# Optimization experiments

Measured on AMD Instinct MI355X. Metric: run time of the kernel, lower is better.

Reference implementation:

```python
import jax, jax.numpy as jnp
import numpy as np
from math import sqrt

D_MODEL = 512
HEADS = 8
D_K = D_MODEL // HEADS
DIM_FFN = 2048
EPS = 1e-6


def setup_inputs() -> dict:
    key = jax.random.key(0)
    ks = jax.random.split(key, 16)
    b, s = 2, 256
    inp = {
        "x": jax.random.normal(ks[0], (b, s, D_MODEL), dtype=jnp.float32),
        "connection_bias_k": jax.random.normal(ks[1], (b, s, s, D_MODEL), dtype=jnp.float32) * 0.02,
        "connection_bias_v": jax.random.normal(ks[2], (b, s, s, D_MODEL), dtype=jnp.float32) * 0.02,
        "mask": jnp.zeros((b, s), dtype=jnp.int32),
        "Wq": jax.random.normal(ks[3], (D_MODEL, D_MODEL), dtype=jnp.float32) / sqrt(D_MODEL),
        "bq": jnp.zeros((D_MODEL,), dtype=jnp.float32),
        "Wk": jax.random.normal(ks[4], (D_MODEL, D_MODEL), dtype=jnp.float32) / sqrt(D_MODEL),
        "bk": jnp.zeros((D_MODEL,), dtype=jnp.float32),
        "Wv": jax.random.normal(ks[5], (D_MODEL, D_MODEL), dtype=jnp.float32) / sqrt(D_MODEL),
        "bv": jnp.zeros((D_MODEL,), dtype=jnp.float32),
        "Wo": jax.random.normal(ks[6], (D_MODEL, D_MODEL), dtype=jnp.float32) / sqrt(D_MODEL),
        "bo": jnp.zeros((D_MODEL,), dtype=jnp.float32),
        "alpha1": jnp.ones((D_MODEL,), dtype=jnp.float32),
        "beta1": jnp.zeros((D_MODEL,), dtype=jnp.float32),
        "alpha2": jnp.ones((D_MODEL,), dtype=jnp.float32),
        "beta2": jnp.zeros((D_MODEL,), dtype=jnp.float32),
        "W1": jax.random.normal(ks[7], (DIM_FFN, D_MODEL), dtype=jnp.float32) / sqrt(D_MODEL),
        "b1": jnp.zeros((DIM_FFN,), dtype=jnp.float32),
        "W2": jax.random.normal(ks[8], (D_MODEL, DIM_FFN), dtype=jnp.float32) / sqrt(DIM_FFN),
        "b2": jnp.zeros((D_MODEL,), dtype=jnp.float32),
    }
    return inp


def _norm(x, alpha, beta):
    # torch .std() is unbiased (ddof=1); note std is added to eps OUTSIDE variance
    mu = jnp.mean(x, axis=-1, keepdims=True)
    sd = jnp.std(x, axis=-1, ddof=1, keepdims=True)
    return alpha * (x - mu) / (sd + EPS) + beta


def reference(x, connection_bias_k, connection_bias_v, mask,
              Wq, bq, Wk, bk, Wv, bv, Wo, bo,
              alpha1, beta1, alpha2, beta2, W1, b1, W2, b2):
    b, s, _ = x.shape
    h, dk = HEADS, D_K

    x2 = _norm(x, alpha1, beta1)
    # projections -> [b, h, s, dk]
    q = (x2 @ Wq.T + bq).reshape(b, s, h, dk).transpose(0, 2, 1, 3)
    k = (x2 @ Wk.T + bk).reshape(b, s, h, dk).transpose(0, 2, 1, 3)
    v = (x2 @ Wv.T + bv).reshape(b, s, h, dk).transpose(0, 2, 1, 3)

    # biases reshaped to (b, s1, s2, h, dk); biased_k[b,h,i,j] = k[b,h,j] + bias[b,j,i,h]
    bk_r = connection_bias_k.reshape(b, s, s, h, dk)
    bv_r = connection_bias_v.reshape(b, s, s, h, dk)

    # scores[b,h,i,j] = q_i . (k_j + bias_k[b,j,i,h]) / sqrt(dk)
    scores = (jnp.einsum('bhid,bhjd->bhij', q, k)
              + jnp.einsum('bhid,bjihd->bhij', q, bk_r)) / sqrt(dk)

    # mask [b,s] -> [b,1,s,1], broadcast over heads and key dim (matches torch)
    m = mask[:, None, :, None]
    scores = jnp.where(m == 1, -1e9, scores)
    attn = jax.nn.softmax(scores, axis=-1)

    # out[b,h,i,d] = sum_j attn[b,h,i,j] * (v[b,h,j] + bias_v[b,j,i,h])
    out = (jnp.einsum('bhij,bhjd->bhid', attn, v)
           + jnp.einsum('bhij,bjihd->bhid', attn, bv_r))
    concat = out.transpose(0, 2, 1, 3).reshape(b, s, D_MODEL)
    attn_out = concat @ Wo.T + bo

    x = x + attn_out
    x2 = _norm(x, alpha2, beta2)
    ff = jax.nn.relu(x2 @ W1.T + b1) @ W2.T + b2
    return x + ff
```

## Files before the change

kernel.cpp:

```cpp
#include <hip/hip_runtime.h>
#include <math.h>

#define D_MODEL 512
#define NHEADS 8
#define DK 64
#define DFFN 2048

typedef __attribute__((ext_vector_type(8))) __bf16 bf16x8;
typedef __attribute__((ext_vector_type(4))) float floatx4;
typedef __attribute__((ext_vector_type(4))) float fvec4;

__global__ __launch_bounds__(256) void ln_kernel(
    const float* __restrict__ x, const float* __restrict__ alpha,
    const float* __restrict__ beta, __bf16* __restrict__ y) {
  int w = threadIdx.x >> 6, lane = threadIdx.x & 63;
  int row = blockIdx.x * 4 + w;
  const float* xr = x + (size_t)row * D_MODEL + lane * 8;
  fvec4 v0 = *(const fvec4*)xr;
  fvec4 v1 = *(const fvec4*)(xr + 4);
  float sm = v0.x + v0.y + v0.z + v0.w + v1.x + v1.y + v1.z + v1.w;
  float qd = v0.x * v0.x + v0.y * v0.y + v0.z * v0.z + v0.w * v0.w +
             v1.x * v1.x + v1.y * v1.y + v1.z * v1.z + v1.w * v1.w;
  for (int m = 1; m < 64; m <<= 1) {
    sm += __shfl_xor(sm, m);
    qd += __shfl_xor(qd, m);
  }
  float mu = sm * (1.0f / D_MODEL);
  float var = (qd - (float)D_MODEL * mu * mu) * (1.0f / (D_MODEL - 1));
  float inv = 1.0f / (sqrtf(fmaxf(var, 0.0f)) + 1e-6f);
  fvec4 a0 = *(const fvec4*)(alpha + lane * 8);
  fvec4 a1 = *(const fvec4*)(alpha + lane * 8 + 4);
  fvec4 b0 = *(const fvec4*)(beta + lane * 8);
  fvec4 b1 = *(const fvec4*)(beta + lane * 8 + 4);
  union { __bf16 h[8]; uint4 u4; } pk;
  pk.h[0] = (__bf16)(a0.x * (v0.x - mu) * inv + b0.x);
  pk.h[1] = (__bf16)(a0.y * (v0.y - mu) * inv + b0.y);
  pk.h[2] = (__bf16)(a0.z * (v0.z - mu) * inv + b0.z);
  pk.h[3] = (__bf16)(a0.w * (v0.w - mu) * inv + b0.w);
  pk.h[4] = (__bf16)(a1.x * (v1.x - mu) * inv + b1.x);
  pk.h[5] = (__bf16)(a1.y * (v1.y - mu) * inv + b1.y);
  pk.h[6] = (__bf16)(a1.z * (v1.z - mu) * inv + b1.z);
  pk.h[7] = (__bf16)(a1.w * (v1.w - mu) * inv + b1.w);
  *(uint4*)(y + (size_t)row * D_MODEL + lane * 8) = pk.u4;
}

struct Seg { const float* src; __bf16* dst; int n4; };
struct Segs6 { Seg s[6]; };
__global__ __launch_bounds__(256) void cast7(Segs6 cs,
    const float* __restrict__ bq, const float* __restrict__ bk,
    const float* __restrict__ bv, float* __restrict__ bqkv) {
  if (blockIdx.y == 6) {
    int idx = blockIdx.x * 256 + threadIdx.x;
    if (idx < 3 * D_MODEL) {
      float v = idx < 512 ? bq[idx] : (idx < 1024 ? bk[idx - 512] : bv[idx - 1024]);
      bqkv[idx] = v;
    }
    return;
  }
  Seg sg = cs.s[blockIdx.y];
  int stride = gridDim.x * 256;
  for (int idx = blockIdx.x * 256 + threadIdx.x; idx < sg.n4; idx += stride) {
    float4 f = ((const float4*)sg.src)[idx];
    union { __bf16 h[4]; uint2 u; } pk;
    pk.h[0] = (__bf16)f.x; pk.h[1] = (__bf16)f.y;
    pk.h[2] = (__bf16)f.z; pk.h[3] = (__bf16)f.w;
    ((uint2*)sg.dst)[idx] = pk.u;
  }
}

template <int RELU, int OUT_BF16>
__global__ __launch_bounds__(64) void wave_gemm(
    const __bf16* __restrict__ A, int lda, const __bf16* __restrict__ B, int ldb,
    const float* __restrict__ bias, const float* __restrict__ res,
    void* __restrict__ Cv, int N, int K) {
  int lane = threadIdx.x;
  int r16 = lane & 15;
  int ko = (lane >> 4) * 8;
  int m0 = blockIdx.y * 32, n0 = blockIdx.x * 32;
  const __bf16* A0 = A + (size_t)(m0 + r16) * lda + ko;
  const __bf16* A1 = A0 + (size_t)16 * lda;
  const __bf16* B0 = B + (size_t)(n0 + r16) * ldb + ko;
  const __bf16* B1 = B0 + (size_t)16 * ldb;
  floatx4 acc00 = {0.f, 0.f, 0.f, 0.f};
  floatx4 acc01 = acc00, acc10 = acc00, acc11 = acc00;
#pragma unroll 4
  for (int k0 = 0; k0 < K; k0 += 32) {
    bf16x8 a0 = *(const bf16x8*)(A0 + k0);
    bf16x8 a1 = *(const bf16x8*)(A1 + k0);
    bf16x8 b0 = *(const bf16x8*)(B0 + k0);
    bf16x8 b1 = *(const bf16x8*)(B1 + k0);
    acc00 = __builtin_amdgcn_mfma_f32_16x16x32_bf16(a0, b0, acc00, 0, 0, 0);
    acc01 = __builtin_amdgcn_mfma_f32_16x16x32_bf16(a0, b1, acc01, 0, 0, 0);
    acc10 = __builtin_amdgcn_mfma_f32_16x16x32_bf16(a1, b0, acc10, 0, 0, 0);
    acc11 = __builtin_amdgcn_mfma_f32_16x16x32_bf16(a1, b1, acc11, 0, 0, 0);
  }
  int col = lane & 15, rb = (lane >> 4) * 4;
  floatx4 accs[2][2] = {{acc00, acc01}, {acc10, acc11}};
#pragma unroll
  for (int i = 0; i < 2; ++i) {
#pragma unroll
    for (int j = 0; j < 2; ++j) {
#pragma unroll
      for (int r = 0; r < 4; ++r) {
        int row = m0 + i * 16 + rb + r;
        int cc = n0 + j * 16 + col;
        float v = accs[i][j][r] + bias[cc];
        if (res) v += res[(size_t)row * N + cc];
        if (RELU) v = fmaxf(v, 0.0f);
        if (OUT_BF16)
          ((__bf16*)Cv)[(size_t)row * N + cc] = (__bf16)v;
        else
          ((float*)Cv)[(size_t)row * N + cc] = v;
      }
    }
  }
}

__global__ __launch_bounds__(512) void attn_kernel(
    const float* __restrict__ qkv, int ldq,
    const float* __restrict__ cbk, const float* __restrict__ cbv,
    const int* __restrict__ mask, __bf16* __restrict__ concat, int s) {
  int i = blockIdx.x % s;
  int b = blockIdx.x / s;
  int t = threadIdx.x;
  int w = t >> 6;
  int lane = t & 63;
  int h = lane >> 3;

  __shared__ float sc[NHEADS][257];
  __shared__ float sums[NHEADS];
  __shared__ float part[8][D_MODEL];

  size_t tok_i = (size_t)(b * s + i);
  const float* qp = qkv + tok_i * ldq + lane * 8;
  fvec4 q0 = *(const fvec4*)(qp);
  fvec4 q1 = *(const fvec4*)(qp + 4);

  const float* kb  = qkv + (size_t)(b * s) * ldq + 512 + lane * 8;
  const float* cbb = cbk + ((size_t)b * s * s + i) * (size_t)D_MODEL + lane * 8;

#pragma unroll 4
  for (int jj = 0; jj < 32; ++jj) {
    int j = w * 32 + jj;
    const float* kp = kb + (size_t)j * ldq;
    const float* cp = cbb + (size_t)j * s * D_MODEL;
    fvec4 k0 = *(const fvec4*)(kp);
    fvec4 k1 = *(const fvec4*)(kp + 4);
    fvec4 c0 = __builtin_nontemporal_load((const fvec4*)cp);
    fvec4 c1 = __builtin_nontemporal_load(((const fvec4*)cp) + 1);
    float d = q0.x * (k0.x + c0.x) + q0.y * (k0.y + c0.y) +
              q0.z * (k0.z + c0.z) + q0.w * (k0.w + c0.w) +
              q1.x * (k1.x + c1.x) + q1.y * (k1.y + c1.y) +
              q1.z * (k1.z + c1.z) + q1.w * (k1.w + c1.w);
    d += __shfl_xor(d, 1);
    d += __shfl_xor(d, 2);
    d += __shfl_xor(d, 4);
    if ((lane & 7) == 0) sc[h][j] = d * 0.125f;
  }
  __syncthreads();

  {
    bool masked = (mask[b * s + i] == 1);
    float vals[4];
    float mx = -1e30f;
#pragma unroll
    for (int kk = 0; kk < 4; ++kk) {
      float xv = sc[w][lane + kk * 64];
      if (masked) xv = -1e9f;
      vals[kk] = xv;
      mx = fmaxf(mx, xv);
    }
    for (int m = 1; m < 64; m <<= 1) mx = fmaxf(mx, __shfl_xor(mx, m));
    float ls = 0.f;
#pragma unroll
    for (int kk = 0; kk < 4; ++kk) {
      float e = expf(vals[kk] - mx);
      sc[w][lane + kk * 64] = e;
      ls += e;
    }
    for (int m = 1; m < 64; m <<= 1) ls += __shfl_xor(ls, m);
    if (lane == 0) sums[w] = ls;
  }
  __syncthreads();

  fvec4 a0 = {0.f, 0.f, 0.f, 0.f};
  fvec4 a1 = {0.f, 0.f, 0.f, 0.f};
  const float* vb  = qkv + (size_t)(b * s) * ldq + 1024 + lane * 8;
  const float* cvb = cbv + ((size_t)b * s * s + i) * (size_t)D_MODEL + lane * 8;
#pragma unroll 4
  for (int jj = 0; jj < 32; ++jj) {
    int j = w * 32 + jj;
    const float* vp = vb + (size_t)j * ldq;
    const float* cp = cvb + (size_t)j * s * D_MODEL;
    fvec4 v0 = *(const fvec4*)(vp);
    fvec4 v1 = *(const fvec4*)(vp + 4);
    fvec4 c0 = __builtin_nontemporal_load((const fvec4*)cp);
    fvec4 c1 = __builtin_nontemporal_load(((const fvec4*)cp) + 1);
    float pj = sc[h][j];
    a0.x += pj * (v0.x + c0.x); a0.y += pj * (v0.y + c0.y);
    a0.z += pj * (v0.z + c0.z); a0.w += pj * (v0.w + c0.w);
    a1.x += pj * (v1.x + c1.x); a1.y += pj * (v1.y + c1.y);
    a1.z += pj * (v1.z + c1.z); a1.w += pj * (v1.w + c1.w);
  }
  *(fvec4*)&part[w][lane * 8] = a0;
  *(fvec4*)&part[w][lane * 8 + 4] = a1;
  __syncthreads();

  if (t < 256) {
    int d0 = t * 2;
    float inv = 1.0f / sums[d0 >> 6];
    float o0 = 0.f, o1 = 0.f;
#pragma unroll
    for (int ww = 0; ww < 8; ++ww) {
      o0 += part[ww][d0];
      o1 += part[ww][d0 + 1];
    }
    union { __bf16 h2[2]; unsigned int u; } pk;
    pk.h2[0] = (__bf16)(o0 * inv);
    pk.h2[1] = (__bf16)(o1 * inv);
    *(unsigned int*)(concat + tok_i * D_MODEL + d0) = pk.u;
  }
}

extern "C" void kernel_launch(void* const* d_in, const int* in_sizes, int n_in,
                              void* d_out, int out_size, void* d_ws, size_t ws_size,
                              hipStream_t stream) {
  const float* x      = (const float*)d_in[0];
  const float* cbk    = (const float*)d_in[1];
  const float* cbv    = (const float*)d_in[2];
  const int*   mask   = (const int*)d_in[3];
  const float* Wq     = (const float*)d_in[4];
  const float* bq     = (const float*)d_in[5];
  const float* Wk     = (const float*)d_in[6];
  const float* bk     = (const float*)d_in[7];
  const float* Wv     = (const float*)d_in[8];
  const float* bv     = (const float*)d_in[9];
  const float* Wo     = (const float*)d_in[10];
  const float* bo     = (const float*)d_in[11];
  const float* alpha1 = (const float*)d_in[12];
  const float* beta1  = (const float*)d_in[13];
  const float* alpha2 = (const float*)d_in[14];
  const float* beta2  = (const float*)d_in[15];
  const float* W1     = (const float*)d_in[16];
  const float* b1     = (const float*)d_in[17];
  const float* W2     = (const float*)d_in[18];
  const float* b2     = (const float*)d_in[19];

  int bs = in_sizes[0] / D_MODEL;
  int s  = in_sizes[1] / in_sizes[0];

  char* wp = (char*)d_ws;
  auto carve = [&](size_t bytes) {
    char* p = wp;
    wp += (bytes + 255) & ~(size_t)255;
    return p;
  };
  __bf16* x2    = (__bf16*)carve((size_t)bs * D_MODEL * 2);
  __bf16* wqkv  = (__bf16*)carve((size_t)3 * D_MODEL * D_MODEL * 2);
  __bf16* wo_b  = (__bf16*)carve((size_t)D_MODEL * D_MODEL * 2);
  __bf16* w1_b  = (__bf16*)carve((size_t)DFFN * D_MODEL * 2);
  __bf16* w2_b  = (__bf16*)carve((size_t)D_MODEL * DFFN * 2);
  float*  bqkv  = (float*)carve((size_t)3 * D_MODEL * 4);
  float*  qkv   = (float*)carve((size_t)bs * 3 * D_MODEL * 4);
  __bf16* conc  = (__bf16*)carve((size_t)bs * D_MODEL * 2);
  float*  xres  = (float*)carve((size_t)bs * D_MODEL * 4);
  __bf16* x2b   = (__bf16*)carve((size_t)bs * D_MODEL * 2);
  __bf16* f1    = (__bf16*)carve((size_t)bs * DFFN * 2);

  Segs6 cs;
  cs.s[0] = {Wq, wqkv,                 D_MODEL * D_MODEL / 4};
  cs.s[1] = {Wk, wqkv + D_MODEL * D_MODEL,     D_MODEL * D_MODEL / 4};
  cs.s[2] = {Wv, wqkv + 2 * D_MODEL * D_MODEL, D_MODEL * D_MODEL / 4};
  cs.s[3] = {Wo, wo_b, D_MODEL * D_MODEL / 4};
  cs.s[4] = {W1, w1_b, DFFN * D_MODEL / 4};
  cs.s[5] = {W2, w2_b, D_MODEL * DFFN / 4};
  cast7<<<dim3(256, 7), 256, 0, stream>>>(cs, bq, bk, bv, bqkv);

  ln_kernel<<<bs / 4, 256, 0, stream>>>(x, alpha1, beta1, x2);

  wave_gemm<0, 0><<<dim3(3 * D_MODEL / 32, bs / 32), 64, 0, stream>>>(
      x2, D_MODEL, wqkv, D_MODEL, bqkv, nullptr, qkv, 3 * D_MODEL, D_MODEL);

  attn_kernel<<<bs, 512, 0, stream>>>(qkv, 3 * D_MODEL, cbk, cbv, mask, conc, s);

  wave_gemm<0, 0><<<dim3(D_MODEL / 32, bs / 32), 64, 0, stream>>>(
      conc, D_MODEL, wo_b, D_MODEL, bo, x, xres, D_MODEL, D_MODEL);

  ln_kernel<<<bs / 4, 256, 0, stream>>>(xres, alpha2, beta2, x2b);

  wave_gemm<1, 1><<<dim3(DFFN / 32, bs / 32), 64, 0, stream>>>(
      x2b, D_MODEL, w1_b, D_MODEL, b1, nullptr, f1, DFFN, D_MODEL);

  wave_gemm<0, 0><<<dim3(D_MODEL / 32, bs / 32), 64, 0, stream>>>(
      f1, DFFN, w2_b, DFFN, b2, xres, d_out, D_MODEL, DFFN);
}
```

Measured before the change: 621.6 us.

## Fuse LN1 into the weight-cast prep kernel and LN2 into the Wo GEMM

The first LayerNorm becomes an extra grid slice of the weight/bias cast kernel, which removes one launch. The Wo output-projection GEMM plus residual is fused with the second LayerNorm in a new kernel. Each 512-thread block there computes a full 32-row strip across all 512 columns, stages it in shared memory, and normalizes it in place. This cuts a launch and a round trip of xres, but the Wo GEMM now runs on only 16 blocks, so it has much less parallelism than the previous 256 wave-sized blocks.

```diff
diff --git a/kernel.cpp b/kernel.cpp
--- a/kernel.cpp
+++ b/kernel.cpp
@@ -10,46 +10,49 @@
 typedef __attribute__((ext_vector_type(4))) float floatx4;
 typedef __attribute__((ext_vector_type(4))) float fvec4;
 
-__global__ __launch_bounds__(256) void ln_kernel(
-    const float* __restrict__ x, const float* __restrict__ alpha,
-    const float* __restrict__ beta, __bf16* __restrict__ y) {
-  int w = threadIdx.x >> 6, lane = threadIdx.x & 63;
-  int row = blockIdx.x * 4 + w;
-  const float* xr = x + (size_t)row * D_MODEL + lane * 8;
-  fvec4 v0 = *(const fvec4*)xr;
-  fvec4 v1 = *(const fvec4*)(xr + 4);
-  float sm = v0.x + v0.y + v0.z + v0.w + v1.x + v1.y + v1.z + v1.w;
-  float qd = v0.x * v0.x + v0.y * v0.y + v0.z * v0.z + v0.w * v0.w +
-             v1.x * v1.x + v1.y * v1.y + v1.z * v1.z + v1.w * v1.w;
-  for (int m = 1; m < 64; m <<= 1) {
-    sm += __shfl_xor(sm, m);
-    qd += __shfl_xor(qd, m);
-  }
-  float mu = sm * (1.0f / D_MODEL);
-  float var = (qd - (float)D_MODEL * mu * mu) * (1.0f / (D_MODEL - 1));
-  float inv = 1.0f / (sqrtf(fmaxf(var, 0.0f)) + 1e-6f);
-  fvec4 a0 = *(const fvec4*)(alpha + lane * 8);
-  fvec4 a1 = *(const fvec4*)(alpha + lane * 8 + 4);
-  fvec4 b0 = *(const fvec4*)(beta + lane * 8);
-  fvec4 b1 = *(const fvec4*)(beta + lane * 8 + 4);
-  union { __bf16 h[8]; uint4 u4; } pk;
-  pk.h[0] = (__bf16)(a0.x * (v0.x - mu) * inv + b0.x);
-  pk.h[1] = (__bf16)(a0.y * (v0.y - mu) * inv + b0.y);
-  pk.h[2] = (__bf16)(a0.z * (v0.z - mu) * inv + b0.z);
-  pk.h[3] = (__bf16)(a0.w * (v0.w - mu) * inv + b0.w);
-  pk.h[4] = (__bf16)(a1.x * (v1.x - mu) * inv + b1.x);
-  pk.h[5] = (__bf16)(a1.y * (v1.y - mu) * inv + b1.y);
-  pk.h[6] = (__bf16)(a1.z * (v1.z - mu) * inv + b1.z);
-  pk.h[7] = (__bf16)(a1.w * (v1.w - mu) * inv + b1.w);
-  *(uint4*)(y + (size_t)row * D_MODEL + lane * 8) = pk.u4;
-}
-
 struct Seg { const float* src; __bf16* dst; int n4; };
 struct Segs6 { Seg s[6]; };
-__global__ __launch_bounds__(256) void cast7(Segs6 cs,
+
+__global__ __launch_bounds__(256) void prep(Segs6 cs,
     const float* __restrict__ bq, const float* __restrict__ bk,
-    const float* __restrict__ bv, float* __restrict__ bqkv) {
-  if (blockIdx.y == 6) {
+    const float* __restrict__ bv, float* __restrict__ bqkv,
+    const float* __restrict__ x, const float* __restrict__ alpha,
+    const float* __restrict__ beta, __bf16* __restrict__ y_out, int rows) {
+  int y = blockIdx.y;
+  if (y == 7) {
+    if (blockIdx.x >= (rows >> 2)) return;
+    int w = threadIdx.x >> 6, lane = threadIdx.x & 63;
+    int row = blockIdx.x * 4 + w;
+    const float* xr = x + (size_t)row * D_MODEL + lane * 8;
+    fvec4 v0 = *(const fvec4*)xr;
+    fvec4 v1 = *(const fvec4*)(xr + 4);
+    float sm = v0.x + v0.y + v0.z + v0.w + v1.x + v1.y + v1.z + v1.w;
+    float qd = v0.x * v0.x + v0.y * v0.y + v0.z * v0.z + v0.w * v0.w +
+               v1.x * v1.x + v1.y * v1.y + v1.z * v1.z + v1.w * v1.w;
+    for (int m = 1; m < 64; m <<= 1) {
+      sm += __shfl_xor(sm, m);
+      qd += __shfl_xor(qd, m);
+    }
+    float mu = sm * (1.0f / D_MODEL);
+    float var = (qd - (float)D_MODEL * mu * mu) * (1.0f / (D_MODEL - 1));
+    float inv = 1.0f / (sqrtf(fmaxf(var, 0.0f)) + 1e-6f);
+    fvec4 a0 = *(const fvec4*)(alpha + lane * 8);
+    fvec4 a1 = *(const fvec4*)(alpha + lane * 8 + 4);
+    fvec4 b0 = *(const fvec4*)(beta + lane * 8);
+    fvec4 b1 = *(const fvec4*)(beta + lane * 8 + 4);
+    union { __bf16 h[8]; uint4 u4; } pk;
+    pk.h[0] = (__bf16)(a0.x * (v0.x - mu) * inv + b0.x);
+    pk.h[1] = (__bf16)(a0.y * (v0.y - mu) * inv + b0.y);
+    pk.h[2] = (__bf16)(a0.z * (v0.z - mu) * inv + b0.z);
+    pk.h[3] = (__bf16)(a0.w * (v0.w - mu) * inv + b0.w);
+    pk.h[4] = (__bf16)(a1.x * (v1.x - mu) * inv + b1.x);
+    pk.h[5] = (__bf16)(a1.y * (v1.y - mu) * inv + b1.y);
+    pk.h[6] = (__bf16)(a1.z * (v1.z - mu) * inv + b1.z);
+    pk.h[7] = (__bf16)(a1.w * (v1.w - mu) * inv + b1.w);
+    *(uint4*)(y_out + (size_t)row * D_MODEL + lane * 8) = pk.u4;
+    return;
+  }
+  if (y == 6) {
     int idx = blockIdx.x * 256 + threadIdx.x;
     if (idx < 3 * D_MODEL) {
       float v = idx < 512 ? bq[idx] : (idx < 1024 ? bk[idx - 512] : bv[idx - 1024]);
@@ -57,7 +60,7 @@
     }
     return;
   }
-  Seg sg = cs.s[blockIdx.y];
+  Seg sg = cs.s[y];
   int stride = gridDim.x * 256;
   for (int idx = blockIdx.x * 256 + threadIdx.x; idx < sg.n4; idx += stride) {
     float4 f = ((const float4*)sg.src)[idx];
@@ -116,6 +119,84 @@
   }
 }
 
+__global__ __launch_bounds__(512) void wo_ln(
+    const __bf16* __restrict__ conc, const __bf16* __restrict__ Wo,
+    const float* __restrict__ bo, const float* __restrict__ x,
+    const float* __restrict__ alpha, const float* __restrict__ beta,
+    float* __restrict__ xres, __bf16* __restrict__ x2b) {
+  constexpr int LW = D_MODEL + 4;
+  __shared__ float sm[32][LW];
+  int t = threadIdx.x, w = t >> 6, lane = t & 63;
+  int bm = blockIdx.x * 32;
+  int r16 = lane & 15, ko = (lane >> 4) * 8;
+  const __bf16* A0 = conc + (size_t)(bm + r16) * D_MODEL + ko;
+  const __bf16* A1 = A0 + (size_t)16 * D_MODEL;
+  int n0 = w * 64;
+  const __bf16* B0 = Wo + (size_t)(n0 + r16) * D_MODEL + ko;
+  floatx4 acc[2][4];
+#pragma unroll
+  for (int i = 0; i < 2; ++i)
+#pragma unroll
+    for (int jc = 0; jc < 4; ++jc) acc[i][jc] = {0.f, 0.f, 0.f, 0.f};
+#pragma unroll 4
+  for (int k0 = 0; k0 < D_MODEL; k0 += 32) {
+    bf16x8 a0 = *(const bf16x8*)(A0 + k0);
+    bf16x8 a1 = *(const bf16x8*)(A1 + k0);
+#pragma unroll
+    for (int jc = 0; jc < 4; ++jc) {
+      bf16x8 b = *(const bf16x8*)(B0 + (size_t)jc * 16 * D_MODEL + k0);
+      acc[0][jc] = __builtin_amdgcn_mfma_f32_16x16x32_bf16(a0, b, acc[0][jc], 0, 0, 0);
+      acc[1][jc] = __builtin_amdgcn_mfma_f32_16x16x32_bf16(a1, b, acc[1][jc], 0, 0, 0);
+    }
+  }
+  int col = lane & 15, rb = (lane >> 4) * 4;
+#pragma unroll
+  for (int i = 0; i < 2; ++i) {
+#pragma unroll
+    for (int jc = 0; jc < 4; ++jc) {
+#pragma unroll
+      for (int r = 0; r < 4; ++r) {
+        int row = i * 16 + rb + r;
+        int cc = n0 + jc * 16 + col;
+        float v = acc[i][jc][r] + bo[cc] + x[(size_t)(bm + row) * D_MODEL + cc];
+        xres[(size_t)(bm + row) * D_MODEL + cc] = v;
+        sm[row][cc] = v;
+      }
+    }
+  }
+  __syncthreads();
+#pragma unroll
+  for (int rr = 0; rr < 4; ++rr) {
+    int row = w * 4 + rr;
+    fvec4 v0 = *(const fvec4*)&sm[row][lane * 8];
+    fvec4 v1 = *(const fvec4*)&sm[row][lane * 8 + 4];
+    float smm = v0.x + v0.y + v0.z + v0.w + v1.x + v1.y + v1.z + v1.w;
+    float qd = v0.x * v0.x + v0.y * v0.y + v0.z * v0.z + v0.w * v0.w +
+               v1.x * v1.x + v1.y * v1.y + v1.z * v1.z + v1.w * v1.w;
+    for (int m = 1; m < 64; m <<= 1) {
+      smm += __shfl_xor(smm, m);
+      qd += __shfl_xor(qd, m);
+    }
+    float mu = smm * (1.0f / D_MODEL);
+    float var = (qd - (float)D_MODEL * mu * mu) * (1.0f / (D_MODEL - 1));
+    float inv = 1.0f / (sqrtf(fmaxf(var, 0.0f)) + 1e-6f);
+    fvec4 a0 = *(const fvec4*)(alpha + lane * 8);
+    fvec4 a1 = *(const fvec4*)(alpha + lane * 8 + 4);
+    fvec4 b0 = *(const fvec4*)(beta + lane * 8);
+    fvec4 b1 = *(const fvec4*)(beta + lane * 8 + 4);
+    union { __bf16 h[8]; uint4 u4; } pk;
+    pk.h[0] = (__bf16)(a0.x * (v0.x - mu) * inv + b0.x);
+    pk.h[1] = (__bf16)(a0.y * (v0.y - mu) * inv + b0.y);
+    pk.h[2] = (__bf16)(a0.z * (v0.z - mu) * inv + b0.z);
+    pk.h[3] = (__bf16)(a0.w * (v0.w - mu) * inv + b0.w);
+    pk.h[4] = (__bf16)(a1.x * (v1.x - mu) * inv + b1.x);
+    pk.h[5] = (__bf16)(a1.y * (v1.y - mu) * inv + b1.y);
+    pk.h[6] = (__bf16)(a1.z * (v1.z - mu) * inv + b1.z);
+    pk.h[7] = (__bf16)(a1.w * (v1.w - mu) * inv + b1.w);
+    *(uint4*)(x2b + (size_t)(bm + row) * D_MODEL + lane * 8) = pk.u4;
+  }
+}
+
 __global__ __launch_bounds__(512) void attn_kernel(
     const float* __restrict__ qkv, int ldq,
     const float* __restrict__ cbk, const float* __restrict__ cbv,
@@ -274,19 +355,15 @@
   cs.s[3] = {Wo, wo_b, D_MODEL * D_MODEL / 4};
   cs.s[4] = {W1, w1_b, DFFN * D_MODEL / 4};
   cs.s[5] = {W2, w2_b, D_MODEL * DFFN / 4};
-  cast7<<<dim3(256, 7), 256, 0, stream>>>(cs, bq, bk, bv, bqkv);
-
-  ln_kernel<<<bs / 4, 256, 0, stream>>>(x, alpha1, beta1, x2);
+  prep<<<dim3(256, 8), 256, 0, stream>>>(cs, bq, bk, bv, bqkv,
+                                         x, alpha1, beta1, x2, bs);
 
   wave_gemm<0, 0><<<dim3(3 * D_MODEL / 32, bs / 32), 64, 0, stream>>>(
       x2, D_MODEL, wqkv, D_MODEL, bqkv, nullptr, qkv, 3 * D_MODEL, D_MODEL);
 
   attn_kernel<<<bs, 512, 0, stream>>>(qkv, 3 * D_MODEL, cbk, cbv, mask, conc, s);
 
-  wave_gemm<0, 0><<<dim3(D_MODEL / 32, bs / 32), 64, 0, stream>>>(
-      conc, D_MODEL, wo_b, D_MODEL, bo, x, xres, D_MODEL, D_MODEL);
-
-  ln_kernel<<<bs / 4, 256, 0, stream>>>(xres, alpha2, beta2, x2b);
+  wo_ln<<<bs / 32, 512, 0, stream>>>(conc, wo_b, bo, x, alpha2, beta2, xres, x2b);
 
   wave_gemm<1, 1><<<dim3(DFFN / 32, bs / 32), 64, 0, stream>>>(
       x2b, D_MODEL, w1_b, D_MODEL, b1, nullptr, f1, DFFN, D_MODEL);
```

Result: no change. 632.9 us (+1.8%).
